# Kernel optimization log

Measured on AMD Instinct MI355X. Metric: run time of the kernel, lower is better.

Reference implementation:

```python
import jax, jax.numpy as jnp
import numpy as np

TWO_PI = 2.0 * np.pi


def _fftfreq(n, d):
    # numpy-compatible fftfreq, trace/grad-safe in d: [0..n/2-1, -n/2..-1]/(n*d)
    k = jnp.arange(n)
    k = jnp.where(k < (n + 1) // 2, k, k - n).astype(jnp.float32)
    return k / (n * d)


def _forward(x, wp1_re, wp1_im, wp2_re, wp2_im, wr_re, wr_im, ty, tx):
    wp1 = (wp1_re + 1j * wp1_im).astype(jnp.complex64)   # [Ci,Co,m1]
    wp2 = (wp2_re + 1j * wp2_im).astype(jnp.complex64)   # [Ci,Co,m2]
    wr = (wr_re + 1j * wr_im).astype(jnp.complex64)      # [Ci,Co,m1,m2]
    Ny, Nx = x.shape[-2], x.shape[-1]
    dty = ty[1] - ty[0]
    dtx = tx[1] - tx[0]

    alpha = jnp.fft.fft2(x, axes=(-2, -1))               # [B,Ci,Ny,Nx] complex
    lam1 = (1j * TWO_PI * _fftfreq(Ny, dty)).astype(jnp.complex64)  # [Ny]
    lam2 = (1j * TWO_PI * _fftfreq(Nx, dtx)).astype(jnp.complex64)  # [Nx]

    # Pole-residue transfer function factors: Hw = wr / ((lam1-p1)(lam2-p2))
    A1 = 1.0 / (lam1 - wp1[..., None])                   # [Ci,Co,m1,Ny]
    A2 = 1.0 / (lam2 - wp2[..., None])                   # [Ci,Co,m2,Nx]

    # sum over poles (p,q) of Hw -> [Ci,Co,Ny,Nx]
    Hsum = jnp.einsum('ikpq,ikpo,ikqx->ikox', wr, A1, A2)
    res1 = jnp.einsum('biox,ikox->bkox', alpha, Hsum)    # [B,Co,Ny,Nx]
    # sum over frequency grid (o,x) -> residue coefficients [B,Co,m1,m2]
    res2 = jnp.einsum('biox,ikpq,ikpo,ikqx->bkpq', alpha, wr, A1, A2)

    x1 = jnp.real(jnp.fft.ifft2(res1, s=(Ny, Nx), axes=(-2, -1)))

    # explicit pole-exponential evaluation over the spatial grid
    E1 = jnp.exp(wp1[..., None] * ty.astype(jnp.complex64))  # [Ci,Co,m1,Ny]
    E2 = jnp.exp(wp2[..., None] * tx.astype(jnp.complex64))  # [Ci,Co,m2,Nx]
    # res2 channel dim contracts against E1/E2's first (in==out required)
    x2 = jnp.real(jnp.einsum('kbpq,bipz,biqx->kizx', res2, E1, E2)) / (Nx * Ny)
    return x1 + x2


def setup_inputs() -> dict:
    key = jax.random.key(0)
    B, Ci, Co, Ny, Nx, m1, m2 = 8, 32, 32, 128, 128, 4, 5
    ks = jax.random.split(key, 7)
    scale = 1.0 / (Ci * Co)
    x = jax.random.normal(ks[0], (B, Ci, Ny, Nx), jnp.float32)
    wp1_re = scale * jax.random.uniform(ks[1], (Ci, Co, m1), jnp.float32)
    wp1_im = scale * jax.random.uniform(ks[2], (Ci, Co, m1), jnp.float32)
    wp2_re = scale * jax.random.uniform(ks[3], (Ci, Co, m2), jnp.float32)
    wp2_im = scale * jax.random.uniform(ks[4], (Ci, Co, m2), jnp.float32)
    wr_re = scale * jax.random.uniform(ks[5], (Ci, Co, m1, m2), jnp.float32)
    wr_im = scale * jax.random.uniform(ks[6], (Ci, Co, m1, m2), jnp.float32)
    ty = (jnp.arange(Ny) / Ny).astype(jnp.float32)
    tx = (jnp.arange(Nx) / Nx).astype(jnp.float32)
    return dict(x=x, wp1_re=wp1_re, wp1_im=wp1_im, wp2_re=wp2_re, wp2_im=wp2_im,
                wr_re=wr_re, wr_im=wr_im, ty=ty, tx=tx)


def reference(x, wp1_re, wp1_im, wp2_re, wp2_im, wr_re, wr_im, ty, tx):
    return _forward(x, wp1_re, wp1_im, wp2_re, wp2_im, wr_re, wr_im, ty, tx)
```

## Files before the change

kernel.cpp:

```cpp
#include <hip/hip_runtime.h>
#include <math.h>

#define N 128
#define B 8
#define CI 32
#define CO 32
#define M1 4
#define M2 5
#define IK (CI*CO)
#define IKP (IK*M1)
#define IKQ (IK*M2)
#define TWO_PI_F 6.2831853071795864769f

__device__ __forceinline__ float2 cmul(float2 a, float2 b){
    return make_float2(fmaf(a.x,b.x,-(a.y*b.y)), fmaf(a.x,b.y,a.y*b.x));
}
__device__ __forceinline__ float2 cmadd(float2 acc, float2 a, float2 b){
    acc.x = fmaf(a.x, b.x, fmaf(-a.y, b.y, acc.x));
    acc.y = fmaf(a.x, b.y, fmaf( a.y, b.x, acc.y));
    return acc;
}

__global__ void k_A1T(const float* wr_, const float* wi_, const float* t_, float2* A1T){
    int idx = blockIdx.x*256 + threadIdx.x;
    int o   = idx >> 12;
    int ikp = idx & (IKP-1);
    float d = t_[1]-t_[0];
    float invnd = 1.0f/((float)N*d);
    int kk = (o < N/2) ? o : o - N;
    float lam = TWO_PI_F * (float)kk * invnd;
    float dr = -wr_[ikp];
    float di = lam - wi_[ikp];
    float inv = 1.0f/(dr*dr + di*di);
    A1T[idx] = make_float2(dr*inv, -di*inv);
}

__global__ void k_A2(const float* wr_, const float* wi_, const float* t_, float2* A2){
    int idx = blockIdx.x*256 + threadIdx.x;
    int ikq = idx >> 7; int xx = idx & (N-1);
    float d = t_[1]-t_[0];
    float invnd = 1.0f/((float)N*d);
    int kk = (xx < N/2) ? xx : xx - N;
    float lam = TWO_PI_F * (float)kk * invnd;
    float dr = -wr_[ikq];
    float di = lam - wi_[ikq];
    float inv = 1.0f/(dr*dr + di*di);
    A2[idx] = make_float2(dr*inv, -di*inv);
}

__global__ void k_E(const float* wr_, const float* wi_, const float* t_, float2* E){
    int idx = blockIdx.x*256 + threadIdx.x;
    int ikp = idx >> 7; int y = idx & (N-1);
    float t = t_[y];
    float m = expf(wr_[ikp]*t);
    float s, c; sincosf(wi_[ikp]*t, &s, &c);
    E[idx] = make_float2(m*c, m*s);
}

__global__ void k_W2N(const float* wrr, const float* wri, const float2* A2, float2* W2N){
    int idx = blockIdx.x*256 + threadIdx.x;
    int ikp = idx >> 7; int xx = idx & (N-1);
    int ik = ikp >> 2; int p = ikp & 3;
    float2 acc = make_float2(0.f,0.f);
    const float* wr0 = wrr + ik*(M1*M2) + p*M2;
    const float* wi0 = wri + ik*(M1*M2) + p*M2;
    const float2* a2 = A2 + (size_t)ik*(M2*N) + xx;
    #pragma unroll
    for(int q=0;q<M2;q++){
        float2 w = make_float2(wr0[q], wi0[q]);
        acc = cmadd(acc, w, a2[q*N]);
    }
    W2N[(size_t)ikp*N + xx] = acc;
}

template<int SIGNPOS, int REALIN, int SCALE>
__global__ void __launch_bounds__(256) k_fft_rows(const void* in_, float2* out){
    const float sgn = SIGNPOS ? 1.0f : -1.0f;
    __shared__ float tre[16*132];
    __shared__ float tim_[16*132];
    __shared__ float zre[16*136];
    __shared__ float zim[16*136];
    int t = threadIdx.x;
    size_t row0 = (size_t)blockIdx.x * 16;

    if(REALIN){
        const float* src = (const float*)in_ + row0*N;
        #pragma unroll
        for(int j=0;j<8;j++){
            int idx = t + 256*j; int r = idx>>7, cl = idx&127;
            tre[r*132+cl] = src[idx];
        }
    } else {
        const float2* src = (const float2*)in_ + row0*N;
        #pragma unroll
        for(int j=0;j<8;j++){
            int idx = t + 256*j; int r = idx>>7, cl = idx&127;
            float2 v = src[idx];
            tre[r*132+cl] = v.x; tim_[r*132+cl] = v.y;
        }
    }
    float t16c[16], t16s[16];
    #pragma unroll
    for(int j=0;j<16;j++){ float s,c; sincosf(sgn*(TWO_PI_F/16.f)*(float)j, &s,&c); t16c[j]=c; t16s[j]=s; }
    __syncthreads();

    int r = t>>4, u = t&15, b = u&7, h = u>>3;
    float xr[16], xi[16];
    #pragma unroll
    for(int a=0;a<16;a++){
        float vr = tre[r*132 + 8*a + b];
        float vi = REALIN ? 0.f : tim_[r*132 + 8*a + b];
        if(h && (a&1)){ vr = -vr; vi = -vi; }
        xr[a]=vr; xi[a]=vi;
    }
    #pragma unroll
    for(int cc=0; cc<8; cc++){
        float yr=0.f, yi=0.f;
        #pragma unroll
        for(int a=0;a<16;a++){
            int j = (a*cc)&15;
            if(REALIN){
                yr = fmaf(xr[a], t16c[j], yr);
                yi = fmaf(xr[a], t16s[j], yi);
            } else {
                yr = fmaf(xr[a], t16c[j], yr); yr = fmaf(-xi[a], t16s[j], yr);
                yi = fmaf(xr[a], t16s[j], yi); yi = fmaf( xi[a], t16c[j], yi);
            }
        }
        int c = 8*h + cc;
        float s,co; sincosf(sgn*(TWO_PI_F/128.f)*(float)(b*c), &s,&co);
        zre[r*136 + b*17 + c] = fmaf(yr,co,-(yi*s));
        zim[r*136 + b*17 + c] = fmaf(yr,s,  yi*co);
    }
    __syncthreads();

    float t8c[8], t8s[8];
    #pragma unroll
    for(int j=0;j<8;j++){ float s,c; sincosf(sgn*(TWO_PI_F/8.f)*(float)j, &s,&c); t8c[j]=c; t8s[j]=s; }
    int r2 = t>>4, c2 = t&15;
    float zr_[8], zi_[8];
    #pragma unroll
    for(int bb=0;bb<8;bb++){ zr_[bb]=zre[r2*136 + bb*17 + c2]; zi_[bb]=zim[r2*136 + bb*17 + c2]; }
    float2* dst = out + (row0 + r2)*N;
    #pragma unroll
    for(int d=0; d<8; d++){
        float Xr=0.f, Xi=0.f;
        #pragma unroll
        for(int bb=0;bb<8;bb++){
            int j=(bb*d)&7;
            Xr = fmaf(zr_[bb], t8c[j], Xr); Xr = fmaf(-zi_[bb], t8s[j], Xr);
            Xi = fmaf(zr_[bb], t8s[j], Xi); Xi = fmaf( zi_[bb], t8c[j], Xi);
        }
        if(SCALE){ Xr *= (1.f/128.f); Xi *= (1.f/128.f); }
        dst[c2 + 16*d] = make_float2(Xr, Xi);
    }
}

template<int SIGNPOS, int REALOUT, int SCALE>
__global__ void __launch_bounds__(256) k_fft_cols(const float2* in, float2* outc, float* outr){
    const float sgn = SIGNPOS ? 1.0f : -1.0f;
    __shared__ float tre[N*17];
    __shared__ float tim_[N*17];
    __shared__ float zre[8*16*17];
    __shared__ float zim[8*16*17];
    int t = threadIdx.x;
    int img = blockIdx.x >> 3; int x0 = (blockIdx.x & 7)*16;
    const float2* src = in + (size_t)img*N*N + x0;
    #pragma unroll
    for(int j=0;j<8;j++){
        int idx = t + 256*j; int y = idx>>4, xc = idx&15;
        float2 v = src[y*N + xc];
        tre[y*17+xc]=v.x; tim_[y*17+xc]=v.y;
    }
    float t16c[16], t16s[16];
    #pragma unroll
    for(int j=0;j<16;j++){ float s,c; sincosf(sgn*(TWO_PI_F/16.f)*(float)j, &s,&c); t16c[j]=c; t16s[j]=s; }
    __syncthreads();

    int xc = t&15, u = t>>4, b = u&7, h = u>>3;
    float xr[16], xi[16];
    #pragma unroll
    for(int a=0;a<16;a++){
        int y = 8*a + b;
        float vr = tre[y*17+xc];
        float vi = tim_[y*17+xc];
        if(h && (a&1)){ vr = -vr; vi = -vi; }
        xr[a]=vr; xi[a]=vi;
    }
    #pragma unroll
    for(int cc=0; cc<8; cc++){
        float yr=0.f, yi=0.f;
        #pragma unroll
        for(int a=0;a<16;a++){
            int j = (a*cc)&15;
            yr = fmaf(xr[a], t16c[j], yr); yr = fmaf(-xi[a], t16s[j], yr);
            yi = fmaf(xr[a], t16s[j], yi); yi = fmaf( xi[a], t16c[j], yi);
        }
        int c = 8*h + cc;
        float s,co; sincosf(sgn*(TWO_PI_F/128.f)*(float)(b*c), &s,&co);
        zre[(b*16 + c)*17 + xc] = fmaf(yr,co,-(yi*s));
        zim[(b*16 + c)*17 + xc] = fmaf(yr,s,  yi*co);
    }
    __syncthreads();

    float t8c[8], t8s[8];
    #pragma unroll
    for(int j=0;j<8;j++){ float s,c; sincosf(sgn*(TWO_PI_F/8.f)*(float)j, &s,&c); t8c[j]=c; t8s[j]=s; }
    int c2 = t>>4; int x2 = t&15;
    float zr_[8], zi_[8];
    #pragma unroll
    for(int bb=0;bb<8;bb++){ zr_[bb]=zre[(bb*16 + c2)*17 + x2]; zi_[bb]=zim[(bb*16 + c2)*17 + x2]; }
    #pragma unroll
    for(int d=0; d<8; d++){
        float Xr=0.f, Xi=0.f;
        #pragma unroll
        for(int bb=0;bb<8;bb++){
            int j=(bb*d)&7;
            Xr = fmaf(zr_[bb], t8c[j], Xr); Xr = fmaf(-zi_[bb], t8s[j], Xr);
            Xi = fmaf(zr_[bb], t8s[j], Xi); Xi = fmaf( zi_[bb], t8c[j], Xi);
        }
        int ky = c2 + 16*d;
        if(REALOUT){
            outr[(size_t)img*N*N + ky*N + x0 + x2] = Xr * (SCALE ? (1.f/128.f) : 1.f);
        } else {
            if(SCALE){ Xr *= (1.f/128.f); Xi *= (1.f/128.f); }
            outc[(size_t)img*N*N + ky*N + x0 + x2] = make_float2(Xr, Xi);
        }
    }
}

__global__ void __launch_bounds__(256) k_res1(const float2* alpha, const float2* A1T,
                                              const float2* W2N, float2* res1){
    __shared__ float4 At4[B*CI*8];
    int t = threadIdx.x;
    int o  = blockIdx.x >> 3;
    int x0 = (blockIdx.x & 7) * 16;

    {
        int im0 = t >> 3, xq = t & 7;
        #pragma unroll
        for(int j=0;j<8;j++){
            int im = im0 + 32*j;
            At4[im*8 + xq] = *(const float4*)(alpha + (size_t)im*(N*N) + o*N + x0 + 2*xq);
        }
    }
    __syncthreads();

    int k = t >> 3, xh = t & 7;
    float2 acc[B][2];
    #pragma unroll
    for(int b=0;b<B;b++){ acc[b][0]=make_float2(0.f,0.f); acc[b][1]=make_float2(0.f,0.f); }

    const float2* a1base = A1T + (size_t)o*IKP + k*M1;
    const float2* w2base = W2N + ((size_t)k*M1)*N + x0 + 2*xh;

    #pragma unroll 2
    for(int i=0;i<CI;i++){
        float4 a1a = *(const float4*)(a1base + (size_t)i*128);
        float4 a1b = *(const float4*)(a1base + (size_t)i*128 + 2);
        float2 a1v[M1] = { make_float2(a1a.x,a1a.y), make_float2(a1a.z,a1a.w),
                           make_float2(a1b.x,a1b.y), make_float2(a1b.z,a1b.w) };
        float2 h0 = make_float2(0.f,0.f), h1 = make_float2(0.f,0.f);
        const float2* w2 = w2base + (size_t)i*(128*N);
        #pragma unroll
        for(int p=0;p<M1;p++){
            float4 wv = *(const float4*)(w2 + (size_t)p*N);
            h0 = cmadd(h0, a1v[p], make_float2(wv.x,wv.y));
            h1 = cmadd(h1, a1v[p], make_float2(wv.z,wv.w));
        }
        #pragma unroll
        for(int b=0;b<B;b++){
            float4 av = At4[(b*CI + i)*8 + xh];
            acc[b][0] = cmadd(acc[b][0], make_float2(av.x,av.y), h0);
            acc[b][1] = cmadd(acc[b][1], make_float2(av.z,av.w), h1);
        }
    }

    #pragma unroll
    for(int b=0;b<B;b++){
        float4 v = make_float4(acc[b][0].x, acc[b][0].y, acc[b][1].x, acc[b][1].y);
        *(float4*)(res1 + (size_t)(b*CO + k)*(N*N) + o*N + x0 + 2*xh) = v;
    }
}

__global__ void __launch_bounds__(256) k_S_res2(const float2* alpha, const float2* A2,
                                                const float2* A1T, const float* wrr,
                                                const float* wri, float2* res2){
    __shared__ float2 tile[128*17];
    __shared__ float2 A2c[16*80];
    int t = threadIdx.x;
    int ol = t & 15;
    int kl = t >> 4;
    int bid = blockIdx.x;
    int kh = bid & 1;
    int i  = (bid >> 1) & (CI-1);
    int b  = bid >> 6;
    int k0 = kh*16;
    int k  = k0 + kl;
    int ik = i*CO + k;
    const float2* asrc = alpha + ((size_t)(b*CI + i))*(N*N);

    const int trow = t >> 4, txc = t & 15;
    int a2dst[5]; size_t a2src[5];
    #pragma unroll
    for(int s=0;s<5;s++){
        int e = t + 256*s;
        int xcs = e / 80, rs = e - xcs*80;
        int kk = rs / 5, qq = rs - kk*5;
        a2dst[s] = xcs*80 + rs;
        a2src[s] = ((size_t)(i*CO + k0 + kk)*M2 + qq)*N + xcs;
    }

    float2 U[8][5];
    #pragma unroll
    for(int oi=0;oi<8;oi++)
        #pragma unroll
        for(int q=0;q<5;q++) U[oi][q] = make_float2(0.f,0.f);

    float2 pre[8], a2pre[5];
    #pragma unroll
    for(int j=0;j<8;j++) pre[j] = asrc[(trow + 16*j)*N + txc];
    #pragma unroll
    for(int s=0;s<5;s++) a2pre[s] = A2[a2src[s]];

    for(int c=0; c<8; c++){
        __syncthreads();
        #pragma unroll
        for(int j=0;j<8;j++) tile[(trow + 16*j)*17 + txc] = pre[j];
        #pragma unroll
        for(int s=0;s<5;s++) A2c[a2dst[s]] = a2pre[s];
        if(c < 7){
            int x0n = (c+1)*16;
            #pragma unroll
            for(int j=0;j<8;j++) pre[j] = asrc[(trow + 16*j)*N + x0n + txc];
            #pragma unroll
            for(int s=0;s<5;s++) a2pre[s] = A2[a2src[s] + x0n];
        }
        __syncthreads();
        #pragma unroll 2
        for(int xc=0; xc<16; xc++){
            float2 a2v[5];
            const float2* a2row = A2c + xc*80 + kl*5;
            #pragma unroll
            for(int q=0;q<5;q++) a2v[q] = a2row[q];
            #pragma unroll
            for(int oi=0;oi<8;oi++){
                float2 av = tile[(ol + 16*oi)*17 + xc];
                #pragma unroll
                for(int q=0;q<5;q++) U[oi][q] = cmadd(U[oi][q], av, a2v[q]);
            }
        }
    }

    float2 S[4][5];
    #pragma unroll
    for(int p=0;p<4;p++)
        #pragma unroll
        for(int q=0;q<5;q++) S[p][q] = make_float2(0.f,0.f);
    #pragma unroll
    for(int oi=0;oi<8;oi++){
        int o = ol + 16*oi;
        const float2* a1 = A1T + (size_t)o*IKP + (size_t)ik*M1;
        float2 a1v[4];
        #pragma unroll
        for(int p=0;p<4;p++) a1v[p] = a1[p];
        #pragma unroll
        for(int p=0;p<4;p++)
            #pragma unroll
            for(int q=0;q<5;q++) S[p][q] = cmadd(S[p][q], a1v[p], U[oi][q]);
    }
    #pragma unroll
    for(int m=1;m<16;m<<=1){
        #pragma unroll
        for(int p=0;p<4;p++)
            #pragma unroll
            for(int q=0;q<5;q++){
                S[p][q].x += __shfl_xor(S[p][q].x, m);
                S[p][q].y += __shfl_xor(S[p][q].y, m);
            }
    }
    if(ol==0){
        const float* wr0 = wrr + ik*(M1*M2);
        const float* wi0 = wri + ik*(M1*M2);
        float2* dst = res2 + (size_t)(b*CO + k)*(M1*M2);
        #pragma unroll
        for(int p=0;p<4;p++)
            #pragma unroll
            for(int q=0;q<5;q++){
                float2 w = make_float2(wr0[p*5+q], wi0[p*5+q]);
                float2 v = cmul(w, S[p][q]);
                atomicAdd(&dst[p*5+q].x, v.x);
                atomicAdd(&dst[p*5+q].y, v.y);
            }
    }
}

__global__ void __launch_bounds__(256) k_x2(const float2* res2, const float2* E1,
                                            const float2* E2, float* out){
    __shared__ __align__(16) float2 res2s[CI*M1*M2];
    __shared__ __align__(16) float2 Wt[M1*N];
    __shared__ __align__(16) float2 buf[2][M1*N + M2*N];
    int t = threadIdx.x;
    int j  = blockIdx.x & (CO-1);
    int b  = blockIdx.x >> 5;
    int xt = t & 15, yt = t >> 4;

    {
        const float4* s4 = (const float4*)(res2 + (size_t)b*CO*M1*M2);
        float4* d4 = (float4*)res2s;
        d4[t] = s4[t];
        if(t < 64) d4[256+t] = s4[256+t];
    }

    const bool ok2 = (t < 64);
    int pp0 = t >> 6, rem0 = (t & 63) << 1;
    int off0 = pp0*N + rem0,          dst0 = pp0*128 + rem0;
    int qq1 = t >> 6, xi1 = (t & 63) << 1;
    int off1 = qq1*N + xi1,           dst1 = 512 + qq1*128 + xi1;
    int xi2 = (t & 63) << 1;
    int off2 = 4*N + xi2,             dst2 = 512 + 4*128 + xi2;

    const float2* E1c = E1 + ((size_t)j*M1)*N;
    const float2* E2c = E2 + ((size_t)j*M2)*N;

    float4 pre0 = *(const float4*)(E1c + off0);
    float4 pre1 = *(const float4*)(E2c + off1);
    float4 pre2 = ok2 ? *(const float4*)(E2c + off2) : make_float4(0.f,0.f,0.f,0.f);
    *(float4*)(&buf[0][dst0]) = pre0;
    *(float4*)(&buf[0][dst1]) = pre1;
    if(ok2) *(float4*)(&buf[0][dst2]) = pre2;
    int cur = 0;
    __syncthreads();

    float acc[8][8];
    #pragma unroll
    for(int yy=0;yy<8;yy++)
        #pragma unroll
        for(int s=0;s<8;s++) acc[yy][s] = 0.f;

    for(int c=0; c<CI; c++){
        const float2* E2s = buf[cur] + 512;
        #pragma unroll
        for(int s=0;s<2;s++){
            int e = t + 256*s;
            int pp = e >> 7, xi = e & 127;
            const float2* rr = res2s + c*(M1*M2) + pp*M2;
            float2 w = make_float2(0.f,0.f);
            #pragma unroll
            for(int q=0;q<M2;q++) w = cmadd(w, rr[q], E2s[q*128 + xi]);
            Wt[pp*128 + xi] = w;
        }
        if(c+1 < CI){
            E1c += (size_t)CO*M1*N;
            E2c += (size_t)CO*M2*N;
            pre0 = *(const float4*)(E1c + off0);
            pre1 = *(const float4*)(E2c + off1);
            if(ok2) pre2 = *(const float4*)(E2c + off2);
        }
        __syncthreads();

        const float2* E1s = buf[cur];
        #pragma unroll
        for(int p=0;p<4;p++){
            float2 e1[8];
            #pragma unroll
            for(int g=0;g<4;g++){
                float4 a = *(const float4*)(E1s + p*128 + yt*8 + 2*g);
                e1[2*g]   = make_float2(a.x,a.y);
                e1[2*g+1] = make_float2(a.z,a.w);
            }
            #pragma unroll
            for(int s=0;s<4;s++){
                float4 wv = *(const float4*)(Wt + p*128 + 32*s + 2*xt);
                #pragma unroll
                for(int yy=0;yy<8;yy++){
                    float2 e = e1[yy];
                    acc[yy][2*s]   = fmaf(e.x, wv.x, fmaf(-e.y, wv.y, acc[yy][2*s]));
                    acc[yy][2*s+1] = fmaf(e.x, wv.z, fmaf(-e.y, wv.w, acc[yy][2*s+1]));
                }
            }
        }
        if(c+1 < CI){
            float2* nb = buf[cur^1];
            *(float4*)(nb + dst0) = pre0;
            *(float4*)(nb + dst1) = pre1;
            if(ok2) *(float4*)(nb + dst2) = pre2;
        }
        cur ^= 1;
        __syncthreads();
    }

    const float sc = 1.0f/((float)N*(float)N);
    size_t base = (size_t)(b*CO + j)*(N*N);
    #pragma unroll
    for(int yy=0;yy<8;yy++){
        float* orow = out + base + (size_t)(yt*8 + yy)*N;
        #pragma unroll
        for(int s=0;s<4;s++){
            float2* dst = (float2*)(orow + 32*s + 2*xt);
            float2 old = *dst;
            *dst = make_float2(old.x + acc[yy][2*s]*sc, old.y + acc[yy][2*s+1]*sc);
        }
    }
}

extern "C" void kernel_launch(void* const* d_in, const int* in_sizes, int n_in,
                              void* d_out, int out_size, void* d_ws, size_t ws_size,
                              hipStream_t stream){
    const float* x    = (const float*)d_in[0];
    const float* wp1r = (const float*)d_in[1];
    const float* wp1i = (const float*)d_in[2];
    const float* wp2r = (const float*)d_in[3];
    const float* wp2i = (const float*)d_in[4];
    const float* wrr  = (const float*)d_in[5];
    const float* wri  = (const float*)d_in[6];
    const float* ty   = (const float*)d_in[7];
    const float* tx   = (const float*)d_in[8];
    float* out = (float*)d_out;
    float2* ws = (float2*)d_ws;

    const size_t NCIMG = (size_t)B*CI*N*N;
    float2* bufA  = ws;
    float2* alpha = bufA  + NCIMG;
    float2* res1  = alpha + NCIMG;
    float2* A1T   = res1  + NCIMG;
    float2* A2    = A1T   + (size_t)N*IKP;
    float2* W2N   = A2    + (size_t)IKQ*N;
    float2* E1    = W2N   + (size_t)N*IKP;
    float2* E2    = E1    + (size_t)IKP*N;
    float2* res2  = E2    + (size_t)IKQ*N;

    k_A1T<<<(N*IKP)/256, 256, 0, stream>>>(wp1r, wp1i, ty, A1T);
    k_E  <<<(IKP*N)/256, 256, 0, stream>>>(wp1r, wp1i, ty, E1);
    k_A2 <<<(IKQ*N)/256, 256, 0, stream>>>(wp2r, wp2i, tx, A2);
    k_E  <<<(IKQ*N)/256, 256, 0, stream>>>(wp2r, wp2i, tx, E2);
    k_W2N<<<(IKP*N)/256, 256, 0, stream>>>(wrr, wri, A2, W2N);

    k_fft_rows<0,1,0><<<(B*CI*N)/16, 256, 0, stream>>>((const void*)x, bufA);
    k_fft_cols<0,0,0><<<B*CI*8, 256, 0, stream>>>(bufA, alpha, nullptr);

    hipMemsetAsync(res2, 0, (size_t)B*CO*M1*M2*sizeof(float2), stream);
    k_res1<<<N*8, 256, 0, stream>>>(alpha, A1T, W2N, res1);
    k_S_res2<<<B*CI*2, 256, 0, stream>>>(alpha, A2, A1T, wrr, wri, res2);

    k_fft_rows<1,0,1><<<(B*CO*N)/16, 256, 0, stream>>>((const void*)res1, bufA);
    k_fft_cols<1,1,1><<<B*CO*8, 256, 0, stream>>>(bufA, nullptr, out);
    k_x2<<<B*CO, 256, 0, stream>>>(res2, E1, E2, out);
}
```

Measured before the change: 331.2 us.

## Split res2 kernel over output rows and replace atomics with a reduction kernel

```diff
diff --git a/kernel.cpp b/kernel.cpp
--- a/kernel.cpp
+++ b/kernel.cpp
@@ -283,56 +283,53 @@
     }
 }
 
-__global__ void __launch_bounds__(256) k_S_res2(const float2* alpha, const float2* A2,
-                                                const float2* A1T, const float* wrr,
-                                                const float* wri, float2* res2){
-    __shared__ float2 tile[128*17];
-    __shared__ float2 A2c[16*80];
+__global__ void __launch_bounds__(512) k_S_res2(const float2* alpha, const float2* A2,
+                                                const float2* A1T, float2* part){
+    __shared__ float2 tile[64*17];
+    __shared__ float2 A2c[16*160];
     int t = threadIdx.x;
     int ol = t & 15;
     int kl = t >> 4;
     int bid = blockIdx.x;
-    int kh = bid & 1;
+    int oh = bid & 1;
     int i  = (bid >> 1) & (CI-1);
     int b  = bid >> 6;
-    int k0 = kh*16;
-    int k  = k0 + kl;
-    int ik = i*CO + k;
-    const float2* asrc = alpha + ((size_t)(b*CI + i))*(N*N);
+    int ik = i*CO + kl;
+    const float2* asrc = alpha + ((size_t)(b*CI + i))*(N*N) + (size_t)oh*64*N;
 
     const int trow = t >> 4, txc = t & 15;
     int a2dst[5]; size_t a2src[5];
     #pragma unroll
     for(int s=0;s<5;s++){
-        int e = t + 256*s;
-        int xcs = e / 80, rs = e - xcs*80;
+        int e = t + 512*s;
+        int xcs = e / 160, rs = e - xcs*160;
         int kk = rs / 5, qq = rs - kk*5;
-        a2dst[s] = xcs*80 + rs;
-        a2src[s] = ((size_t)(i*CO + k0 + kk)*M2 + qq)*N + xcs;
-    }
-
-    float2 U[8][5];
-    #pragma unroll
-    for(int oi=0;oi<8;oi++)
+        a2dst[s] = xcs*160 + rs;
+        a2src[s] = ((size_t)(i*CO + kk)*M2 + qq)*N + xcs;
+    }
+
+    float2 U[4][5];
+    #pragma unroll
+    for(int oi=0;oi<4;oi++)
         #pragma unroll
         for(int q=0;q<5;q++) U[oi][q] = make_float2(0.f,0.f);
 
-    float2 pre[8], a2pre[5];
-    #pragma unroll
-    for(int j=0;j<8;j++) pre[j] = asrc[(trow + 16*j)*N + txc];
+    float2 pre[2], a2pre[5];
+    #pragma unroll
+    for(int j=0;j<2;j++) pre[j] = asrc[(trow + 32*j)*N + txc];
     #pragma unroll
     for(int s=0;s<5;s++) a2pre[s] = A2[a2src[s]];
 
     for(int c=0; c<8; c++){
         __syncthreads();
         #pragma unroll
-        for(int j=0;j<8;j++) tile[(trow + 16*j)*17 + txc] = pre[j];
+        for(int j=0;j<2;j++) tile[(trow + 32*j)*17 + txc] = pre[j];
         #pragma unroll
         for(int s=0;s<5;s++) A2c[a2dst[s]] = a2pre[s];
         if(c < 7){
             int x0n = (c+1)*16;
             #pragma unroll
-            for(int j=0;j<8;j++) pre[j] = asrc[(trow + 16*j)*N + x0n + txc];
+            for(int j=0;j<2;j++) pre[j] = asrc[(trow + 32*j)*N + x0n + txc];
             #pragma unroll
             for(int s=0;s<5;s++) a2pre[s] = A2[a2src[s] + x0n];
         }
@@ -340,11 +337,11 @@
         #pragma unroll 2
         for(int xc=0; xc<16; xc++){
             float2 a2v[5];
-            const float2* a2row = A2c + xc*80 + kl*5;
+            const float2* a2row = A2c + xc*160 + kl*5;
             #pragma unroll
             for(int q=0;q<5;q++) a2v[q] = a2row[q];
             #pragma unroll
-            for(int oi=0;oi<8;oi++){
+            for(int oi=0;oi<4;oi++){
                 float2 av = tile[(ol + 16*oi)*17 + xc];
                 #pragma unroll
                 for(int q=0;q<5;q++) U[oi][q] = cmadd(U[oi][q], av, a2v[q]);
@@ -358,8 +355,8 @@
         #pragma unroll
         for(int q=0;q<5;q++) S[p][q] = make_float2(0.f,0.f);
     #pragma unroll
-    for(int oi=0;oi<8;oi++){
-        int o = ol + 16*oi;
+    for(int oi=0;oi<4;oi++){
+        int o = oh*64 + ol + 16*oi;
         const float2* a1 = A1T + (size_t)o*IKP + (size_t)ik*M1;
         float2 a1v[4];
         #pragma unroll
@@ -380,19 +377,27 @@
             }
     }
     if(ol==0){
-        const float* wr0 = wrr + ik*(M1*M2);
-        const float* wi0 = wri + ik*(M1*M2);
-        float2* dst = res2 + (size_t)(b*CO + k)*(M1*M2);
+        float2* dst = part + ((size_t)((b*CO + kl)*CI + i)*2 + oh)*(M1*M2);
         #pragma unroll
         for(int p=0;p<4;p++)
             #pragma unroll
-            for(int q=0;q<5;q++){
-                float2 w = make_float2(wr0[p*5+q], wi0[p*5+q]);
-                float2 v = cmul(w, S[p][q]);
-                atomicAdd(&dst[p*5+q].x, v.x);
-                atomicAdd(&dst[p*5+q].y, v.y);
-            }
-    }
+            for(int q=0;q<5;q++) dst[p*5+q] = S[p][q];
+    }
+}
+
+__global__ void k_res2_red(const float2* part, const float* wrr, const float* wri, float2* res2){
+    int idx = blockIdx.x*256 + threadIdx.x;
+    int bk = idx / (M1*M2); int pq = idx - bk*(M1*M2);
+    int k = bk & (CO-1);
+    float2 acc = make_float2(0.f,0.f);
+    for(int i=0;i<CI;i++){
+        int ik = i*CO + k;
+        float2 w = make_float2(wrr[ik*(M1*M2)+pq], wri[ik*(M1*M2)+pq]);
+        const float2* pp = part + ((size_t)(bk*CI+i)*2)*(M1*M2) + pq;
+        float2 s0 = pp[0]; float2 s1 = pp[M1*M2];
+        acc = cmadd(acc, w, make_float2(s0.x+s1.x, s0.y+s1.y));
+    }
+    res2[idx] = acc;
 }
 
 __global__ void __launch_bounds__(256) k_x2(const float2* res2, const float2* E1,
@@ -529,6 +534,7 @@
     float2* E1    = W2N   + (size_t)N*IKP;
     float2* E2    = E1    + (size_t)IKP*N;
     float2* res2  = E2    + (size_t)IKQ*N;
+    float2* part  = res2  + (size_t)B*CO*M1*M2;
 
     k_A1T<<<(N*IKP)/256, 256, 0, stream>>>(wp1r, wp1i, ty, A1T);
     k_E  <<<(IKP*N)/256, 256, 0, stream>>>(wp1r, wp1i, ty, E1);
@@ -539,9 +545,9 @@
     k_fft_rows<0,1,0><<<(B*CI*N)/16, 256, 0, stream>>>((const void*)x, bufA);
     k_fft_cols<0,0,0><<<B*CI*8, 256, 0, stream>>>(bufA, alpha, nullptr);
 
-    hipMemsetAsync(res2, 0, (size_t)B*CO*M1*M2*sizeof(float2), stream);
     k_res1<<<N*8, 256, 0, stream>>>(alpha, A1T, W2N, res1);
-    k_S_res2<<<B*CI*2, 256, 0, stream>>>(alpha, A2, A1T, wrr, wri, res2);
+    k_S_res2<<<B*CI*2, 512, 0, stream>>>(alpha, A2, A1T, part);
+    k_res2_red<<<(B*CO*M1*M2)/256, 256, 0, stream>>>(part, wrr, wri, res2);
 
     k_fft_rows<1,0,1><<<(B*CO*N)/16, 256, 0, stream>>>((const void*)res1, bufA);
     k_fft_cols<1,1,1><<<B*CO*8, 256, 0, stream>>>(bufA, nullptr, out);
```

New measurement: 338.4 us. 2.2% more time.
